# Kernel optimization log

Measured on AMD Instinct MI355X. Metric: run time of the kernel, lower is better.

## Reference

```python
import jax, jax.numpy as jnp
import numpy as np

ATT_NORM = 4.0
EPS = 1e-12

E, H, C, N = 1000000, 8, 16, 100000


def setup_inputs() -> dict:
    key = jax.random.key(0)
    k1, k2, k3, k4, k5 = jax.random.split(key, 5)
    return {
        "x": jax.random.normal(k1, (E, H, C), dtype=jnp.float32),
        "att_l": jax.random.normal(k2, (1, H, C), dtype=jnp.float32),
        "att_r": jax.random.normal(k3, (1, H, C), dtype=jnp.float32),
        "alpha": jax.random.normal(k4, (E, H, 1), dtype=jnp.float32),
        "index": jax.random.randint(k5, (E,), 0, N, dtype=jnp.int32),
        "num_nodes": N,
    }


def reference(x, att_l, att_r, alpha, index, num_nodes):
    # squared L2 norm of per-edge features: [E, H, 1]
    norm_x = jnp.sum(x * x, axis=-1, keepdims=True)
    # scatter-max per destination node: [N, H, 1]
    max_norm_seg = jax.ops.segment_max(norm_x, index, num_segments=num_nodes)
    # gather back per edge and combine: sqrt(max_norm[index] + norm_x)
    max_norm = jnp.sqrt(max_norm_seg[index] + norm_x)  # [E, H, 1]
    # norm of concatenated attention vectors: ||[att_l, att_r]|| over last dim -> [1, H, 1]
    norm_att = ATT_NORM * jnp.sqrt(
        jnp.sum(att_l * att_l, axis=-1, keepdims=True)
        + jnp.sum(att_r * att_r, axis=-1, keepdims=True)
    )
    return alpha / (norm_att * max_norm + EPS)
```

## Files before the change

### kernel.cpp

```cpp
#include <hip/hip_runtime.h>
#include <math.h>

#define EPSF 1e-12f
#define ATT_NORM_F 4.0f
#define H_DIM 8
#define C_DIM 16
#define N_NODES 100000
#define SEG_WORDS (N_NODES * H_DIM)

typedef float v4f __attribute__((ext_vector_type(4)));

__global__ __launch_bounds__(256) void lip_zero(unsigned* __restrict__ p, int n)
{
    int i = blockIdx.x * 256 + threadIdx.x;
    if (i < n) p[i] = 0u;
}

__global__ __launch_bounds__(256) void lip_pass1(
    const float* __restrict__ x, const int* __restrict__ index,
    float* __restrict__ norm_x, unsigned int* __restrict__ seg, int total )
{
    const int stride = gridDim.x * 256;
    const int s0 = blockIdx.x * 256 + threadIdx.x;
    const int lane = s0 & 3;
    const v4f* x4 = (const v4f*)x;

    #pragma unroll 4
    for (int s = s0; s < total; s += stride) {
        v4f v = __builtin_nontemporal_load(&x4[s]);
        float sum = v.x * v.x + v.y * v.y + v.z * v.z + v.w * v.w;
        sum += __shfl_xor(sum, 1);
        sum += __shfl_xor(sum, 2);
        if (lane == 0) {
            int r = s >> 2;
            norm_x[r] = sum;
            int e = r >> 3;
            int h = r & 7;
            atomicMax(&seg[(size_t)index[e] * H_DIM + h], __float_as_uint(sum));
        }
    }
}

__global__ __launch_bounds__(256) void lip_pass2(
    const float* __restrict__ norm_x, const float* __restrict__ alpha,
    const int* __restrict__ index, const unsigned int* __restrict__ seg,
    const float* __restrict__ att_l, const float* __restrict__ att_r,
    float* __restrict__ out, int total)
{
    __shared__ float s_natt[H_DIM];
    int t = threadIdx.x;
    if (t < H_DIM) {
        float s = 0.f;
        #pragma unroll
        for (int c = 0; c < C_DIM; ++c) {
            float l = att_l[t * C_DIM + c];
            float r = att_r[t * C_DIM + c];
            s += l * l + r * r;
        }
        s_natt[t] = ATT_NORM_F * sqrtf(s);
    }
    __syncthreads();

    int tid = blockIdx.x * 256 + t;
    if (tid >= total) return;

    int e    = tid >> 1;
    int half = tid & 1;
    int idx  = index[e];

    const v4f* nx4 = (const v4f*)norm_x;
    const v4f* al4 = (const v4f*)alpha;
    const v4f* sg4 = (const v4f*)seg;

    v4f nx = nx4[tid];
    v4f al = __builtin_nontemporal_load(&al4[tid]);
    v4f sg = sg4[(size_t)idx * 2 + half];

    int h0 = half * 4;
    v4f o;
    o.x = al.x / (s_natt[h0 + 0] * sqrtf(sg.x + nx.x) + EPSF);
    o.y = al.y / (s_natt[h0 + 1] * sqrtf(sg.y + nx.y) + EPSF);
    o.z = al.z / (s_natt[h0 + 2] * sqrtf(sg.z + nx.z) + EPSF);
    o.w = al.w / (s_natt[h0 + 3] * sqrtf(sg.w + nx.w) + EPSF);
    __builtin_nontemporal_store(o, &((v4f*)out)[tid]);
}

__global__ __launch_bounds__(256) void lip_pass2_recompute(
    const float* __restrict__ x, const float* __restrict__ alpha,
    const int* __restrict__ index, const unsigned int* __restrict__ seg,
    const float* __restrict__ att_l, const float* __restrict__ att_r,
    float* __restrict__ out, int rows)
{
    __shared__ float s_natt[H_DIM];
    int t = threadIdx.x;
    if (t < H_DIM) {
        float s = 0.f;
        #pragma unroll
        for (int c = 0; c < C_DIM; ++c) {
            float l = att_l[t * C_DIM + c];
            float r = att_r[t * C_DIM + c];
            s += l * l + r * r;
        }
        s_natt[t] = ATT_NORM_F * sqrtf(s);
    }
    __syncthreads();

    int r = blockIdx.x * blockDim.x + t;
    if (r >= rows) return;

    const float4* x4 = (const float4*)x;
    float s = 0.f;
    #pragma unroll
    for (int q = 0; q < 4; ++q) {
        float4 v = x4[(size_t)r * 4 + q];
        s += v.x * v.x + v.y * v.y + v.z * v.z + v.w * v.w;
    }
    int e = r >> 3;
    int h = r & 7;
    float sg = __uint_as_float(seg[(size_t)index[e] * H_DIM + h]);
    out[r] = alpha[r] / (s_natt[h] * sqrtf(sg + s) + EPSF);
}

__global__ __launch_bounds__(256) void lip_pass1_merged(
    const float* __restrict__ x, const int* __restrict__ index,
    unsigned int* __restrict__ seg, int total )
{
    const int stride = gridDim.x * 256;
    const int s0 = blockIdx.x * 256 + threadIdx.x;
    const int lane = s0 & 3;
    const v4f* x4 = (const v4f*)x;
    #pragma unroll 4
    for (int s = s0; s < total; s += stride) {
        v4f v = __builtin_nontemporal_load(&x4[s]);
        float sum = v.x * v.x + v.y * v.y + v.z * v.z + v.w * v.w;
        sum += __shfl_xor(sum, 1);
        sum += __shfl_xor(sum, 2);
        if (lane == 0) {
            int r = s >> 2;
            int e = r >> 3, h = r & 7;
            atomicMax(&seg[(size_t)index[e] * H_DIM + h], __float_as_uint(sum));
        }
    }
}

extern "C" void kernel_launch(void* const* d_in, const int* in_sizes, int n_in,
                              void* d_out, int out_size, void* d_ws, size_t ws_size,
                              hipStream_t stream) {
    const float* x     = (const float*)d_in[0];
    const float* att_l = (const float*)d_in[1];
    const float* att_r = (const float*)d_in[2];
    const float* alpha = (const float*)d_in[3];
    const int*   index = (const int*)d_in[4];

    const int E    = in_sizes[4];
    const int rows = E * H_DIM;

    size_t seg_pad = ((size_t)SEG_WORDS * 4 + 255) / 256 * 256;
    size_t need    = seg_pad + (size_t)rows * sizeof(float);

    unsigned* seg = (unsigned*)d_ws;
    lip_zero<<<(SEG_WORDS + 255) / 256, 256, 0, stream>>>(seg, SEG_WORDS);

    if (ws_size >= need) {
        float* norm_x = (float*)((char*)d_ws + seg_pad);
        lip_pass1<<<2048, 256, 0, stream>>>(x, index, norm_x, seg, rows * 4);
        int t2 = E * 2;
        lip_pass2<<<(t2 + 255) / 256, 256, 0, stream>>>(
            norm_x, alpha, index, seg, att_l, att_r, (float*)d_out, t2);
    } else {
        lip_pass1_merged<<<2048, 256, 0, stream>>>(x, index, seg, rows * 4);
        lip_pass2_recompute<<<(rows + 255) / 256, 256, 0, stream>>>(
            x, alpha, index, seg, att_l, att_r, (float*)d_out, rows);
    }
}
```

Baseline: 138.4 us.

## Warp-specialize pass1 into producer loads and consumer atomics via shared double buffer

Splits each block of the first pass into three producer wavefronts and one consumer wavefront. The producers stream x, compute the per-row squared norms, store them and stage them in a double-buffered shared array. The consumer wavefront does the index lookup and scatter atomicMax for the previous chunk. The aim is to keep the streaming loads from waiting behind atomic latency, at the cost of a block-wide barrier per chunk and only one wavefront issuing atomics.

```diff
diff --git a/kernel.cpp b/kernel.cpp
--- a/kernel.cpp
+++ b/kernel.cpp
@@ -8,6 +8,9 @@
 #define N_NODES 100000
 #define SEG_WORDS (N_NODES * H_DIM)
 
+#define CHUNK 192
+#define PASSES 4
+
 typedef float v4f __attribute__((ext_vector_type(4)));
 
 __global__ __launch_bounds__(256) void lip_zero(unsigned* __restrict__ p, int n)
@@ -16,28 +19,66 @@
     if (i < n) p[i] = 0u;
 }
 
-__global__ __launch_bounds__(256) void lip_pass1(
+__global__ __launch_bounds__(256) void lip_pass1_pc(
     const float* __restrict__ x, const int* __restrict__ index,
-    float* __restrict__ norm_x, unsigned int* __restrict__ seg, int total )
-{
-    const int stride = gridDim.x * 256;
-    const int s0 = blockIdx.x * 256 + threadIdx.x;
-    const int lane = s0 & 3;
+    float* __restrict__ norm_x, unsigned* __restrict__ seg, int rows)
+{
+    __shared__ float buf[2][CHUNK];
+
+    const int t = threadIdx.x;
+    const int w = t >> 6;
+    const int nchunks = (rows + CHUNK - 1) / CHUNK;
     const v4f* x4 = (const v4f*)x;
 
-    #pragma unroll 4
-    for (int s = s0; s < total; s += stride) {
-        v4f v = __builtin_nontemporal_load(&x4[s]);
-        float sum = v.x * v.x + v.y * v.y + v.z * v.z + v.w * v.w;
-        sum += __shfl_xor(sum, 1);
-        sum += __shfl_xor(sum, 2);
-        if (lane == 0) {
-            int r = s >> 2;
-            norm_x[r] = sum;
-            int e = r >> 3;
-            int h = r & 7;
-            atomicMax(&seg[(size_t)index[e] * H_DIM + h], __float_as_uint(sum));
-        }
+    const int rloc = t >> 2;
+    const int lane = t & 3;
+
+    for (int p = 0; ; ++p) {
+        int c  = blockIdx.x + p * gridDim.x;
+        int cp = c - gridDim.x;
+        bool do_s = (c < nchunks);
+        bool do_a = (p > 0) && (cp < nchunks);
+        if (!do_s && !do_a) break;
+
+        if (w < 3) {
+            if (do_s) {
+                int base = c * CHUNK;
+                float* b = buf[p & 1];
+                #pragma unroll
+                for (int j = 0; j < PASSES; ++j) {
+                    int r = base + j * 48 + rloc;
+                    if (r < rows) {
+                        v4f v = __builtin_nontemporal_load(&x4[(size_t)r * 4 + lane]);
+                        float s = v.x * v.x + v.y * v.y + v.z * v.z + v.w * v.w;
+                        s += __shfl_xor(s, 1);
+                        s += __shfl_xor(s, 2);
+                        if (lane == 0) {
+                            __builtin_nontemporal_store(s, &norm_x[r]);
+                            b[j * 48 + rloc] = s;
+                        }
+                    }
+                }
+            }
+        } else {
+            if (do_a) {
+                int base = cp * CHUNK;
+                const float* b = buf[(p & 1) ^ 1];
+                int ln = t & 63;
+                #pragma unroll
+                for (int k = 0; k < 3; ++k) {
+                    int i = k * 64 + ln;
+                    int r = base + i;
+                    if (r < rows) {
+                        float s = b[i];
+                        int e = r >> 3;
+                        int h = r & 7;
+                        atomicMax(&seg[(size_t)index[e] * H_DIM + h],
+                                  __float_as_uint(s));
+                    }
+                }
+            }
+        }
+        __syncthreads();
     }
 }
 
@@ -83,42 +124,6 @@
     o.z = al.z / (s_natt[h0 + 2] * sqrtf(sg.z + nx.z) + EPSF);
     o.w = al.w / (s_natt[h0 + 3] * sqrtf(sg.w + nx.w) + EPSF);
     __builtin_nontemporal_store(o, &((v4f*)out)[tid]);
-}
-
-__global__ __launch_bounds__(256) void lip_pass2_recompute(
-    const float* __restrict__ x, const float* __restrict__ alpha,
-    const int* __restrict__ index, const unsigned int* __restrict__ seg,
-    const float* __restrict__ att_l, const float* __restrict__ att_r,
-    float* __restrict__ out, int rows)
-{
-    __shared__ float s_natt[H_DIM];
-    int t = threadIdx.x;
-    if (t < H_DIM) {
-        float s = 0.f;
-        #pragma unroll
-        for (int c = 0; c < C_DIM; ++c) {
-            float l = att_l[t * C_DIM + c];
-            float r = att_r[t * C_DIM + c];
-            s += l * l + r * r;
-        }
-        s_natt[t] = ATT_NORM_F * sqrtf(s);
-    }
-    __syncthreads();
-
-    int r = blockIdx.x * blockDim.x + t;
-    if (r >= rows) return;
-
-    const float4* x4 = (const float4*)x;
-    float s = 0.f;
-    #pragma unroll
-    for (int q = 0; q < 4; ++q) {
-        float4 v = x4[(size_t)r * 4 + q];
-        s += v.x * v.x + v.y * v.y + v.z * v.z + v.w * v.w;
-    }
-    int e = r >> 3;
-    int h = r & 7;
-    float sg = __uint_as_float(seg[(size_t)index[e] * H_DIM + h]);
-    out[r] = alpha[r] / (s_natt[h] * sqrtf(sg + s) + EPSF);
 }
 
 __global__ __launch_bounds__(256) void lip_pass1_merged(
@@ -143,6 +148,42 @@
     }
 }
 
+__global__ __launch_bounds__(256) void lip_pass2_recompute(
+    const float* __restrict__ x, const float* __restrict__ alpha,
+    const int* __restrict__ index, const unsigned int* __restrict__ seg,
+    const float* __restrict__ att_l, const float* __restrict__ att_r,
+    float* __restrict__ out, int rows)
+{
+    __shared__ float s_natt[H_DIM];
+    int t = threadIdx.x;
+    if (t < H_DIM) {
+        float s = 0.f;
+        #pragma unroll
+        for (int c = 0; c < C_DIM; ++c) {
+            float l = att_l[t * C_DIM + c];
+            float r = att_r[t * C_DIM + c];
+            s += l * l + r * r;
+        }
+        s_natt[t] = ATT_NORM_F * sqrtf(s);
+    }
+    __syncthreads();
+
+    int r = blockIdx.x * blockDim.x + t;
+    if (r >= rows) return;
+
+    const float4* x4 = (const float4*)x;
+    float s = 0.f;
+    #pragma unroll
+    for (int q = 0; q < 4; ++q) {
+        float4 v = x4[(size_t)r * 4 + q];
+        s += v.x * v.x + v.y * v.y + v.z * v.z + v.w * v.w;
+    }
+    int e = r >> 3;
+    int h = r & 7;
+    float sg = __uint_as_float(seg[(size_t)index[e] * H_DIM + h]);
+    out[r] = alpha[r] / (s_natt[h] * sqrtf(sg + s) + EPSF);
+}
+
 extern "C" void kernel_launch(void* const* d_in, const int* in_sizes, int n_in,
                               void* d_out, int out_size, void* d_ws, size_t ws_size,
                               hipStream_t stream) {
@@ -163,7 +204,7 @@
 
     if (ws_size >= need) {
         float* norm_x = (float*)((char*)d_ws + seg_pad);
-        lip_pass1<<<2048, 256, 0, stream>>>(x, index, norm_x, seg, rows * 4);
+        lip_pass1_pc<<<2048, 256, 0, stream>>>(x, index, norm_x, seg, rows);
         int t2 = E * 2;
         lip_pass2<<<(t2 + 255) / 256, 256, 0, stream>>>(
             norm_x, alpha, index, seg, att_l, att_r, (float*)d_out, t2);
```

New measurement: 132.0 us. 1.05x faster.
